# Kernel tuning notes

Measured on AMD Instinct MI355X. Metric: run time of the kernel, lower is better.

The kernel has to match this reference:

```python
import jax, jax.numpy as jnp
import numpy as np

N, IN_DIM, OUT_DIM, BATCH = 8192, 128, 128, 4


def _glorot(key, shape):
    lim = float(np.sqrt(6.0 / (shape[0] + shape[1])))
    return jax.random.uniform(key, shape, jnp.float32, -lim, lim)


def setup_inputs() -> dict:
    key = jax.random.key(0)
    ks = jax.random.split(key, 16)
    inp = {
        "x": jax.random.normal(ks[0], (BATCH, N, IN_DIM), jnp.float32),
        "L0": jax.random.normal(ks[1], (N, N), jnp.float32) / np.sqrt(N),
        "L1": jax.random.normal(ks[2], (N, N), jnp.float32) / np.sqrt(N),
        "L2": jax.random.normal(ks[3], (N, N), jnp.float32) / np.sqrt(N),
        "L3": jax.random.normal(ks[4], (N, N), jnp.float32) / np.sqrt(N),
    }
    # 8 GCN layers: (branch b, layer l) -> W_bl, bias_bl
    kidx = 5
    for b in range(4):
        for l in range(2):
            d_in = IN_DIM if l == 0 else OUT_DIM
            inp[f"W{b}{l}"] = _glorot(ks[kidx], (d_in, OUT_DIM))
            inp[f"b{b}{l}"] = jnp.zeros((OUT_DIM,), jnp.float32)
            kidx += 1
    return inp


def _gcn_block(L, x, W, b):
    # support = L @ x  (graph propagation), then dense transform + ReLU
    support = jnp.einsum("nm,bmf->bnf", L, x)  # [B, N, F_in]
    return jax.nn.relu(support @ W + b)        # [B, N, F_out]


def reference(x, L0, L1, L2, L3,
              W00, b00, W01, b01,
              W10, b10, W11, b11,
              W20, b20, W21, b21,
              W30, b30, W31, b31):
    x0 = _gcn_block(L0, _gcn_block(L0, x, W00, b00), W01, b01)
    x1 = _gcn_block(L1, _gcn_block(L1, x, W10, b10), W11, b11)
    x2 = _gcn_block(L2, _gcn_block(L2, x, W20, b20), W21, b21)
    x3 = _gcn_block(L3, _gcn_block(L3, x, W30, b30), W31, b31)
    return (x0, x1, x2, x3)
```

## Files before the change

### kernel.cpp

```cpp
#include <hip/hip_runtime.h>
#include <stdint.h>


typedef short bf16x8 __attribute__((ext_vector_type(8)));
typedef float f32x4  __attribute__((ext_vector_type(4)));
typedef float f32x16 __attribute__((ext_vector_type(16)));

static __device__ __forceinline__ unsigned short f2bf(float f) {
  __bf16 h = (__bf16)f;
  return __builtin_bit_cast(unsigned short, h);
}
static __device__ __forceinline__ unsigned int pack2(float a, float b) {
  return (unsigned int)f2bf(a) | ((unsigned int)f2bf(b) << 16);
}
static __device__ __forceinline__ bf16x8 cvt8(float4 lo, float4 hi) {
  bf16x8 r;
  r[0] = (short)f2bf(lo.x); r[1] = (short)f2bf(lo.y);
  r[2] = (short)f2bf(lo.z); r[3] = (short)f2bf(lo.w);
  r[4] = (short)f2bf(hi.x); r[5] = (short)f2bf(hi.y);
  r[6] = (short)f2bf(hi.z); r[7] = (short)f2bf(hi.w);
  return r;
}

#define GLOAD16(g, l)                                                                  \
  __builtin_amdgcn_global_load_lds((const __attribute__((address_space(1))) void*)(g), \
                                   (__attribute__((address_space(3))) void*)(l), 16, 0, 0)

struct WPtrs { const float* w[8]; };
__global__ __launch_bounds__(256)
void prep_w(WPtrs p, unsigned short* __restrict__ wt) {
  const int s = blockIdx.x;
  const float* W = p.w[s];
  unsigned short* dst = wt + s * 16384;
  for (int i = threadIdx.x; i < 16384; i += 256) {
    const int fi = i >> 7, fo = i & 127;
    dst[fo * 128 + fi] = f2bf(W[i]);
  }
}

struct LPtrs { const float* l[4]; };
__global__ __launch_bounds__(256)
void conv_l(LPtrs p, char* __restrict__ lbf) {
  __shared__ char T[65536];
  const int t = threadIdx.x, lane = t & 63, wave = t >> 6;
  const int rg = blockIdx.x, kg = blockIdx.y, br = blockIdx.z;
  const float* L = p.l[br];
  const int r0 = rg * 64, k0 = kg * 512;
  const int mt = rg >> 2, rowoff = (rg & 3) * 64, kt0 = kg * 16;
#pragma unroll
  for (int i = 0; i < 16; ++i) {
    const int rr = wave * 16 + i;
    const float* src = L + (size_t)(r0 + rr) * 8192 + k0;
#pragma unroll
    for (int half = 0; half < 2; ++half) {
      float4 v = ((const float4*)src)[half * 64 + lane];
      const int ktl = half * 8 + (lane >> 3);
      const int ch  = ((lane >> 1) & 3) ^ ((rr >> 1) & 3);
      uint2 pv; pv.x = pack2(v.x, v.y); pv.y = pack2(v.z, v.w);
      *(uint2*)(T + ktl * 4096 + rr * 64 + ch * 16 + (lane & 1) * 8) = pv;
    }
  }
  __syncthreads();
  char* dstb = lbf + ((size_t)(br * 32 + mt) * 256 + kt0) * 16384 + rowoff * 64;
#pragma unroll
  for (int ktl = 0; ktl < 16; ++ktl)
    ((uint4*)(dstb + (size_t)ktl * 16384))[t] = ((const uint4*)(T + ktl * 4096))[t];
}

template <int AFP32>
__global__ __launch_bounds__(256)
void small_gemm(const float* __restrict__ x, const unsigned short* __restrict__ H1m,
                const unsigned short* __restrict__ WT, unsigned short* __restrict__ Z) {
  __shared__ unsigned short Sa[128 * 136];

  const int t = threadIdx.x, lane = t & 63, wave = t >> 6;
  const int l15 = lane & 15, lk = (lane >> 4) * 8;
  const int wm = (wave >> 1) * 64, wn = (wave & 1) * 64;
  const int mt = blockIdx.x, br = blockIdx.y;
  const int batch = mt >> 6, node0 = (mt & 63) * 128;

  {
    const int row = t >> 1, seg = (t & 1) * 64;
    if (AFP32) {
      const float4* src = (const float4*)(x + ((size_t)batch * 8192 + node0 + row) * 128 + seg);
      uint4* dst = (uint4*)&Sa[row * 136 + seg];
#pragma unroll
      for (int i = 0; i < 8; ++i) {
        float4 a = src[i * 2], b = src[i * 2 + 1];
        uint4 v;
        v.x = pack2(a.x, a.y); v.y = pack2(a.z, a.w);
        v.z = pack2(b.x, b.y); v.w = pack2(b.z, b.w);
        dst[i] = v;
      }
    } else {
      const uint4* src = (const uint4*)(H1m + ((size_t)(br * 4 + batch) * 8192 + node0 + row) * 128 + seg);
      uint4* dst = (uint4*)&Sa[row * 136 + seg];
#pragma unroll
      for (int i = 0; i < 8; ++i) dst[i] = src[i];
    }
  }
  __syncthreads();

  const unsigned short* WTb = WT + (size_t)(2 * br + (AFP32 ? 0 : 1)) * 16384;
  f32x4 acc[4][4];
#pragma unroll
  for (int i = 0; i < 4; ++i)
#pragma unroll
    for (int j = 0; j < 4; ++j) acc[i][j] = f32x4{0.f, 0.f, 0.f, 0.f};

#pragma unroll
  for (int kk = 0; kk < 4; ++kk) {
    bf16x8 av[4], wv[4];
#pragma unroll
    for (int mi = 0; mi < 4; ++mi)
      av[mi] = *(const bf16x8*)&Sa[(wm + mi * 16 + l15) * 136 + kk * 32 + lk];
#pragma unroll
    for (int ni = 0; ni < 4; ++ni)
      wv[ni] = *(const bf16x8*)&WTb[(wn + ni * 16 + l15) * 128 + kk * 32 + lk];
#pragma unroll
    for (int mi = 0; mi < 4; ++mi)
#pragma unroll
      for (int ni = 0; ni < 4; ++ni)
        acc[mi][ni] = __builtin_amdgcn_mfma_f32_16x16x32_bf16(av[mi], wv[ni], acc[mi][ni], 0, 0, 0);
  }

#pragma unroll
  for (int mi = 0; mi < 4; ++mi) {
#pragma unroll
    for (int ni = 0; ni < 4; ++ni) {
      const int row0 = wm + mi * 16 + (lane >> 4) * 4;
      const int col  = wn + ni * 16 + l15;
      uint2 pv;
      pv.x = pack2(acc[mi][ni][0], acc[mi][ni][1]);
      pv.y = pack2(acc[mi][ni][2], acc[mi][ni][3]);
      *(uint2*)(Z + ((size_t)br * 512 + batch * 128 + col) * 8192 + node0 + row0) = pv;
    }
  }
}

struct BigArgs {
  const float* L[4];
  const float* bias[4];
  const unsigned short* Z;
  void* Dst;
};

#define DO_MFMA() do {                                                       \
    __builtin_amdgcn_s_setprio(1);                                           \
    c00 = __builtin_amdgcn_mfma_f32_32x32x16_bf16(av0, bv0, c00, 0, 0, 0);   \
    c01 = __builtin_amdgcn_mfma_f32_32x32x16_bf16(av0, bv1, c01, 0, 0, 0);   \
    c10 = __builtin_amdgcn_mfma_f32_32x32x16_bf16(av1, bv0, c10, 0, 0, 0);   \
    c11 = __builtin_amdgcn_mfma_f32_32x32x16_bf16(av1, bv1, c11, 0, 0, 0);   \
    c20 = __builtin_amdgcn_mfma_f32_32x32x16_bf16(av2, bv0, c20, 0, 0, 0);   \
    c21 = __builtin_amdgcn_mfma_f32_32x32x16_bf16(av2, bv1, c21, 0, 0, 0);   \
    c30 = __builtin_amdgcn_mfma_f32_32x32x16_bf16(av3, bv0, c30, 0, 0, 0);   \
    c31 = __builtin_amdgcn_mfma_f32_32x32x16_bf16(av3, bv1, c31, 0, 0, 0);   \
    __builtin_amdgcn_s_setprio(0); } while (0)

#define RD(ab_, bb_, s_) do {                                          \
    const int _ch = ((2 * (s_) + hk) ^ key4) * 16;                     \
    av0 = *(const bf16x8*)((ab_) + aBase + _ch);                       \
    av1 = *(const bf16x8*)((ab_) + aBase + 2048 + _ch);                \
    av2 = *(const bf16x8*)((ab_) + aBase + 4096 + _ch);                \
    av3 = *(const bf16x8*)((ab_) + aBase + 6144 + _ch);                \
    bv0 = *(const bf16x8*)((bb_) + bBase + _ch);                       \
    bv1 = *(const bf16x8*)((bb_) + bBase + 2048 + _ch); } while (0)

#define BIG_EPILOGUE()                                                                     \
  __syncthreads();                                                                          \
  if (LAYER == 0) {                                                                         \
    unsigned short* S16 = (unsigned short*)smem;                                            \
    _Pragma("unroll")                                                                       \
    for (int h = 0; h < 2; ++h) {                                                           \
      if (((wave >> 1) & 1) == h) {                                                         \
        EPI16(0, 0, c00); EPI16(0, 1, c01);                                                 \
        EPI16(1, 0, c10); EPI16(1, 1, c11);                                                 \
        EPI16(2, 0, c20); EPI16(2, 1, c21);                                                 \
        EPI16(3, 0, c30); EPI16(3, 1, c31);                                                 \
      }                                                                                     \
      __syncthreads();                                                                      \
      const int batch = nb * 2 + h;                                                         \
      const int row = t >> 1, seg = (t & 1) * 64;                                           \
      unsigned short* Dst = (unsigned short*)a.Dst;                                         \
      const uint4* src = (const uint4*)&S16[row * 136 + seg];                               \
      uint4* dst = (uint4*)(Dst + ((size_t)(br * 4 + batch) * 8192 + mbase + row) * 128 + seg); \
      _Pragma("unroll") for (int i = 0; i < 8; ++i) dst[i] = src[i];                        \
      __syncthreads();                                                                      \
    }                                                                                       \
  } else {                                                                                  \
    float* S32 = (float*)smem;                                                              \
    _Pragma("unroll")                                                                       \
    for (int h = 0; h < 2; ++h) {                                                           \
      _Pragma("unroll")                                                                     \
      for (int rh = 0; rh < 2; ++rh) {                                                      \
        if (((wave >> 1) & 1) == h && (wave >> 2) == rh) {                                  \
          EPI32(0, 0, c00); EPI32(0, 1, c01);                                               \
          EPI32(1, 0, c10); EPI32(1, 1, c11);                                               \
          EPI32(2, 0, c20); EPI32(2, 1, c21);                                               \
          EPI32(3, 0, c30); EPI32(3, 1, c31);                                               \
        }                                                                                   \
        __syncthreads();                                                                    \
        const int batch = nb * 2 + h;                                                       \
        const int row = t >> 2, seg = (t & 3) * 32;                                         \
        float* Dst = (float*)a.Dst;                                                         \
        const float4* src = (const float4*)&S32[row * 128 + seg];                           \
        float4* dst = (float4*)(Dst + ((size_t)(br * 4 + batch) * 8192 + mbase + rh * 128 + row) * 128 + seg); \
        _Pragma("unroll") for (int i = 0; i < 8; ++i) dst[i] = src[i];                      \
        __syncthreads();                                                                    \
      }                                                                                     \
    }                                                                                       \
  }

#define EPI16(AM, BN, ACC) do {                                             \
    const int col = (wave & 1) * 64 + (BN) * 32 + l31;                      \
    const float bvv = bias[col];                                            \
    _Pragma("unroll") for (int r = 0; r < 16; ++r) {                        \
      const int row = wm + (AM) * 32 + (r & 3) + 8 * (r >> 2) + 4 * hk;     \
      S16[row * 136 + col] = f2bf(fmaxf(ACC[r] + bvv, 0.f));                \
    } } while (0)
#define EPI32(AM, BN, ACC) do {                                             \
    const int col = (wave & 1) * 64 + (BN) * 32 + l31;                      \
    const float bvv = bias[col];                                            \
    _Pragma("unroll") for (int r = 0; r < 16; ++r) {                        \
      const int lrow = (AM) * 32 + (r & 3) + 8 * (r >> 2) + 4 * hk;         \
      S32[lrow * 128 + col] = fmaxf(ACC[r] + bvv, 0.f);                     \
    } } while (0)

template <int LAYER>
__global__ __launch_bounds__(512)
void big_gemm_pc(BigArgs a, const char* __restrict__ Lbf) {
  extern __shared__ char smem[];

  const int t = threadIdx.x, lane = t & 63, wave = t >> 6;
  const int l31 = lane & 31, hk = lane >> 5;
  const int wm = (wave >> 2) * 128, wn = (wave & 3) * 64;

  const int bid = blockIdx.x;
  const int work = (bid & 7) * 32 + (bid >> 3);
  const int nb = work & 1, mt = (work >> 1) & 31, br = work >> 6;
  const int mbase = mt * 256;

  const float* bias = a.bias[br];
  const unsigned short* Zb = a.Z + (size_t)br * (512 * 8192);

  const char* aTiles = Lbf + ((size_t)(br * 32 + mt) * 256) * 16384;
  const unsigned short* bG = Zb + (size_t)(nb * 256 + wave * 32 + (lane >> 2)) * 8192
                                + ((lane & 3) ^ ((lane >> 3) & 3)) * 8;

  const int aBase = (wm + l31) * 64;
  const int bBase = (wn + l31) * 64;
  const int key4 = (l31 >> 1) & 3;

  f32x16 c00{}, c01{}, c10{}, c11{}, c20{}, c21{}, c30{}, c31{};
  bf16x8 av0, av1, av2, av3, bv0, bv1;

#define STG(T_) do {                                                          \
    const char* _as = aTiles + (size_t)(T_) * 16384 + wave * 2048 + lane * 16;\
    char* _ad = smem + ((T_) & 3) * 16384 + wave * 2048;                      \
    GLOAD16(_as, _ad);                                                        \
    GLOAD16(_as + 1024, _ad + 1024);                                          \
    const unsigned short* _bp = bG + (size_t)(T_) * 32;                       \
    char* _bl = smem + 65536 + ((T_) & 3) * 16384 + wave * 2048;              \
    GLOAD16(_bp, _bl);                                                        \
    GLOAD16(_bp + 16 * 8192, _bl + 1024); } while (0)

#define ITER(T_, VMSTR, DO_STG) do {                                          \
    asm volatile("s_waitcnt " VMSTR ::: "memory");                            \
    __builtin_amdgcn_s_barrier();                                             \
    if (DO_STG) STG((T_) + 3);                                                \
    const char* _ab = smem + ((T_) & 3) * 16384;                              \
    const char* _bb = smem + 65536 + ((T_) & 3) * 16384;                      \
    RD(_ab, _bb, 0);                                                          \
    DO_MFMA();                                                                \
    RD(_ab, _bb, 1);                                                          \
    DO_MFMA();                                                                \
  } while (0)

  STG(0); STG(1); STG(2);

  for (int T = 0; T < 252; T += 4) {
    ITER(T,     "vmcnt(8)", 1);
    ITER(T + 1, "vmcnt(8)", 1);
    ITER(T + 2, "vmcnt(8)", 1);
    ITER(T + 3, "vmcnt(8)", 1);
  }
  ITER(252, "vmcnt(8)", 1);
  ITER(253, "vmcnt(8)", 0);
  ITER(254, "vmcnt(4)", 0);
  ITER(255, "vmcnt(0)", 0);
#undef ITER
#undef STG

  BIG_EPILOGUE()
}

template <int LAYER>
__global__ __launch_bounds__(512, 2)
void big_gemm_rs(BigArgs a) {
  extern __shared__ char smem[];

  const int t = threadIdx.x, lane = t & 63, wave = t >> 6;
  const int l31 = lane & 31, hk = lane >> 5;
  const int wm = (wave >> 2) * 128, wn = (wave & 3) * 64;

  const int bid = blockIdx.x;
  const int work = (bid & 7) * 32 + (bid >> 3);
  const int nb = work & 1, mt = (work >> 1) & 31, br = work >> 6;
  const int mbase = mt * 256;

  const float* A = a.L[br];
  const float* bias = a.bias[br];
  const unsigned short* Zb = a.Z + (size_t)br * (512 * 8192);

  const int arow = t >> 1, ah = t & 1;
  const float* aG = A + (size_t)(mbase + arow) * 8192 + ah * 16;
  const int c0 = 2 * ah, akey = (arow >> 1) & 3;
  char* aRowL = smem + arow * 64;
  const unsigned short* bG = Zb + (size_t)(nb * 256 + wave * 32 + (lane >> 2)) * 8192
                                + ((lane & 3) ^ ((lane >> 3) & 3)) * 8;
  char* bWave = smem + 32768 + wave * 2048;

  const int aBase = (wm + l31) * 64;
  const int bBase = (wn + l31) * 64;
  const int key4 = (l31 >> 1) & 3;

  f32x16 c00{}, c01{}, c10{}, c11{}, c20{}, c21{}, c30{}, c31{};
  float4 s0[4], s1[4], s2[4];
  bf16x8 av0, av1, av2, av3, bv0, bv1;

#define GLB(T_) do {                                                   \
    const unsigned short* _bp = bG + (size_t)(T_) * 32;                \
    char* _bl = bWave + ((T_) & 3) * 16384;                            \
    GLOAD16(_bp, _bl);                                                 \
    GLOAD16(_bp + 16 * 8192, _bl + 1024); } while (0)
#define LOADA(T_, R) do {                                              \
    const float* _ap = aG + (size_t)(T_) * 32;                         \
    R[0] = *(const float4*)(_ap);                                      \
    R[1] = *(const float4*)(_ap + 4);                                  \
    R[2] = *(const float4*)(_ap + 8);                                  \
    R[3] = *(const float4*)(_ap + 12); } while (0)
#define WRITEA(T_, R) do {                                             \
    char* _al = aRowL + (((T_) & 1)) * 16384;                          \
    *(bf16x8*)(_al + ((c0 ^ akey) * 16))       = cvt8(R[0], R[1]);     \
    *(bf16x8*)(_al + (((c0 + 1) ^ akey) * 16)) = cvt8(R[2], R[3]); } while (0)
#define ITER(T_, SLOAD, SWRITE, VMSTR, DO_STAGE, DO_WRITE) do {        \
    asm volatile("s_waitcnt " VMSTR ::: "memory");                     \
    asm volatile("s_waitcnt lgkmcnt(0)" ::: "memory");                 \
    __builtin_amdgcn_s_barrier();                                      \
    if (DO_STAGE) { GLB((T_) + 3); LOADA((T_) + 3, SLOAD); }           \
    const char* _ab = smem + ((T_) & 1) * 16384;                       \
    const char* _bb = smem + 32768 + ((T_) & 3) * 16384;               \
    RD(_ab, _bb, 0);                                                   \
    DO_MFMA();                                                         \
    if (DO_WRITE) WRITEA((T_) + 1, SWRITE);                            \
    RD(_ab, _bb, 1);                                                   \
    DO_MFMA();                                                         \
  } while (0)

  GLB(0); LOADA(0, s0);
  GLB(1); LOADA(1, s1);
  GLB(2); LOADA(2, s2);
  WRITEA(0, s0);

  for (int T = 0; T < 252; T += 3) {
    ITER(T,     s0, s1, "vmcnt(12)", 1, 1);
    ITER(T + 1, s1, s2, "vmcnt(12)", 1, 1);
    ITER(T + 2, s2, s0, "vmcnt(12)", 1, 1);
  }
  ITER(252, s0, s1, "vmcnt(12)", 1, 1);
  ITER(253, s0, s2, "vmcnt(12)", 0, 1);
  ITER(254, s0, s0, "vmcnt(6)",  0, 1);
  ITER(255, s0, s0, "vmcnt(0)",  0, 0);
#undef ITER
#undef WRITEA
#undef LOADA
#undef GLB

  BIG_EPILOGUE()
}

extern "C" void kernel_launch(void* const* d_in, const int* in_sizes, int n_in,
                              void* d_out, int out_size, void* d_ws, size_t ws_size,
                              hipStream_t stream) {
  const float* x = (const float*)d_in[0];
  unsigned short* Z   = (unsigned short*)d_ws;
  unsigned short* H1m = Z + (size_t)4 * 512 * 8192;
  unsigned short* WT  = H1m + (size_t)4 * 4 * 8192 * 128;
  char* Lbf = (char*)(WT + 8 * 16384);
  float* out = (float*)d_out;

  const size_t NEED_PC = (size_t)33554432 + 33554432 + 262144 + 536870912;
  const bool use_pc = ws_size >= NEED_PC;

  static int attr_done = 0;
  if (!attr_done) {
    hipFuncSetAttribute((const void*)big_gemm_pc<0>, hipFuncAttributeMaxDynamicSharedMemorySize, 131072);
    hipFuncSetAttribute((const void*)big_gemm_pc<1>, hipFuncAttributeMaxDynamicSharedMemorySize, 131072);
    hipFuncSetAttribute((const void*)big_gemm_rs<0>, hipFuncAttributeMaxDynamicSharedMemorySize, 98304);
    hipFuncSetAttribute((const void*)big_gemm_rs<1>, hipFuncAttributeMaxDynamicSharedMemorySize, 98304);
    attr_done = 1;
  }

  WPtrs wp;
  for (int b = 0; b < 4; ++b) {
    wp.w[b * 2 + 0] = (const float*)d_in[5 + b * 4 + 0];
    wp.w[b * 2 + 1] = (const float*)d_in[5 + b * 4 + 2];
  }
  prep_w<<<8, 256, 0, stream>>>(wp, WT);

  BigArgs a0, a1;
  for (int b = 0; b < 4; ++b) {
    a0.L[b] = (const float*)d_in[1 + b];
    a1.L[b] = (const float*)d_in[1 + b];
    a0.bias[b] = (const float*)d_in[6 + b * 4];
    a1.bias[b] = (const float*)d_in[8 + b * 4];
  }
  a0.Z = Z; a0.Dst = (void*)H1m;
  a1.Z = Z; a1.Dst = (void*)out;

  if (use_pc) {
    LPtrs lp;
    for (int b = 0; b < 4; ++b) lp.l[b] = (const float*)d_in[1 + b];
    conv_l<<<dim3(128, 16, 4), 256, 0, stream>>>(lp, Lbf);
    small_gemm<1><<<dim3(256, 4), 256, 0, stream>>>(x, nullptr, WT, Z);
    big_gemm_pc<0><<<256, 512, 131072, stream>>>(a0, Lbf);
    small_gemm<0><<<dim3(256, 4), 256, 0, stream>>>(nullptr, H1m, WT, Z);
    big_gemm_pc<1><<<256, 512, 131072, stream>>>(a1, Lbf);
  } else {
    small_gemm<1><<<dim3(256, 4), 256, 0, stream>>>(x, nullptr, WT, Z);
    big_gemm_rs<0><<<256, 512, 98304, stream>>>(a0);
    small_gemm<0><<<dim3(256, 4), 256, 0, stream>>>(nullptr, H1m, WT, Z);
    big_gemm_rs<1><<<256, 512, 98304, stream>>>(a1);
  }
}
```

Measured before the change: 934.8 us.

## Shrink L conversion tiles, use nontemporal access, and double-buffer MFMA operand reads

The L fp32-to-bf16 conversion kernel now handles half as many columns per block, with twice as many blocks and half the LDS. It uses nontemporal loads and stores so the streamed L data does not pollute the cache. In the big GEMM kernels, both k-substeps' LDS operands go into separate register sets; in the pc variant both reads are issued before the MFMAs, to hide LDS latency. This costs more VGPRs and may lower occupancy.

```diff
diff --git a/kernel.cpp b/kernel.cpp
--- a/kernel.cpp
+++ b/kernel.cpp
@@ -4,6 +4,7 @@
 
 typedef short bf16x8 __attribute__((ext_vector_type(8)));
 typedef float f32x4  __attribute__((ext_vector_type(4)));
+typedef unsigned int u32x4 __attribute__((ext_vector_type(4)));
 typedef float f32x16 __attribute__((ext_vector_type(16)));
 
 static __device__ __forceinline__ unsigned short f2bf(float f) {
@@ -41,30 +42,29 @@
 struct LPtrs { const float* l[4]; };
 __global__ __launch_bounds__(256)
 void conv_l(LPtrs p, char* __restrict__ lbf) {
-  __shared__ char T[65536];
+  __shared__ char T[32768];
   const int t = threadIdx.x, lane = t & 63, wave = t >> 6;
   const int rg = blockIdx.x, kg = blockIdx.y, br = blockIdx.z;
   const float* L = p.l[br];
-  const int r0 = rg * 64, k0 = kg * 512;
-  const int mt = rg >> 2, rowoff = (rg & 3) * 64, kt0 = kg * 16;
+  const int r0 = rg * 64, k0 = kg * 256;
+  const int mt = rg >> 2, rowoff = (rg & 3) * 64, kt0 = kg * 8;
 #pragma unroll
   for (int i = 0; i < 16; ++i) {
     const int rr = wave * 16 + i;
-    const float* src = L + (size_t)(r0 + rr) * 8192 + k0;
-#pragma unroll
-    for (int half = 0; half < 2; ++half) {
-      float4 v = ((const float4*)src)[half * 64 + lane];
-      const int ktl = half * 8 + (lane >> 3);
-      const int ch  = ((lane >> 1) & 3) ^ ((rr >> 1) & 3);
-      uint2 pv; pv.x = pack2(v.x, v.y); pv.y = pack2(v.z, v.w);
-      *(uint2*)(T + ktl * 4096 + rr * 64 + ch * 16 + (lane & 1) * 8) = pv;
-    }
+    const f32x4* src = (const f32x4*)(L + (size_t)(r0 + rr) * 8192 + k0);
+    f32x4 v = __builtin_nontemporal_load(src + lane);
+    const int ktl = lane >> 3;
+    const int ch  = ((lane >> 1) & 3) ^ ((rr >> 1) & 3);
+    uint2 pv; pv.x = pack2(v[0], v[1]); pv.y = pack2(v[2], v[3]);
+    *(uint2*)(T + ktl * 4096 + rr * 64 + ch * 16 + (lane & 1) * 8) = pv;
   }
   __syncthreads();
   char* dstb = lbf + ((size_t)(br * 32 + mt) * 256 + kt0) * 16384 + rowoff * 64;
 #pragma unroll
-  for (int ktl = 0; ktl < 16; ++ktl)
-    ((uint4*)(dstb + (size_t)ktl * 16384))[t] = ((const uint4*)(T + ktl * 4096))[t];
+  for (int ktl = 0; ktl < 8; ++ktl) {
+    u32x4 v = ((const u32x4*)(T + ktl * 4096))[t];
+    __builtin_nontemporal_store(v, (u32x4*)(dstb + (size_t)ktl * 16384) + t);
+  }
 }
 
 template <int AFP32>
@@ -145,26 +145,26 @@
   void* Dst;
 };
 
-#define DO_MFMA() do {                                                       \
+#define MFMASET(AV0, AV1, AV2, AV3, BV0, BV1) do {                           \
     __builtin_amdgcn_s_setprio(1);                                           \
-    c00 = __builtin_amdgcn_mfma_f32_32x32x16_bf16(av0, bv0, c00, 0, 0, 0);   \
-    c01 = __builtin_amdgcn_mfma_f32_32x32x16_bf16(av0, bv1, c01, 0, 0, 0);   \
-    c10 = __builtin_amdgcn_mfma_f32_32x32x16_bf16(av1, bv0, c10, 0, 0, 0);   \
-    c11 = __builtin_amdgcn_mfma_f32_32x32x16_bf16(av1, bv1, c11, 0, 0, 0);   \
-    c20 = __builtin_amdgcn_mfma_f32_32x32x16_bf16(av2, bv0, c20, 0, 0, 0);   \
-    c21 = __builtin_amdgcn_mfma_f32_32x32x16_bf16(av2, bv1, c21, 0, 0, 0);   \
-    c30 = __builtin_amdgcn_mfma_f32_32x32x16_bf16(av3, bv0, c30, 0, 0, 0);   \
-    c31 = __builtin_amdgcn_mfma_f32_32x32x16_bf16(av3, bv1, c31, 0, 0, 0);   \
+    c00 = __builtin_amdgcn_mfma_f32_32x32x16_bf16(AV0, BV0, c00, 0, 0, 0);   \
+    c01 = __builtin_amdgcn_mfma_f32_32x32x16_bf16(AV0, BV1, c01, 0, 0, 0);   \
+    c10 = __builtin_amdgcn_mfma_f32_32x32x16_bf16(AV1, BV0, c10, 0, 0, 0);   \
+    c11 = __builtin_amdgcn_mfma_f32_32x32x16_bf16(AV1, BV1, c11, 0, 0, 0);   \
+    c20 = __builtin_amdgcn_mfma_f32_32x32x16_bf16(AV2, BV0, c20, 0, 0, 0);   \
+    c21 = __builtin_amdgcn_mfma_f32_32x32x16_bf16(AV2, BV1, c21, 0, 0, 0);   \
+    c30 = __builtin_amdgcn_mfma_f32_32x32x16_bf16(AV3, BV0, c30, 0, 0, 0);   \
+    c31 = __builtin_amdgcn_mfma_f32_32x32x16_bf16(AV3, BV1, c31, 0, 0, 0);   \
     __builtin_amdgcn_s_setprio(0); } while (0)
 
-#define RD(ab_, bb_, s_) do {                                          \
+#define RDSET(ab_, bb_, s_, AV0, AV1, AV2, AV3, BV0, BV1) do {         \
     const int _ch = ((2 * (s_) + hk) ^ key4) * 16;                     \
-    av0 = *(const bf16x8*)((ab_) + aBase + _ch);                       \
-    av1 = *(const bf16x8*)((ab_) + aBase + 2048 + _ch);                \
-    av2 = *(const bf16x8*)((ab_) + aBase + 4096 + _ch);                \
-    av3 = *(const bf16x8*)((ab_) + aBase + 6144 + _ch);                \
-    bv0 = *(const bf16x8*)((bb_) + bBase + _ch);                       \
-    bv1 = *(const bf16x8*)((bb_) + bBase + 2048 + _ch); } while (0)
+    AV0 = *(const bf16x8*)((ab_) + aBase + _ch);                       \
+    AV1 = *(const bf16x8*)((ab_) + aBase + 2048 + _ch);                \
+    AV2 = *(const bf16x8*)((ab_) + aBase + 4096 + _ch);                \
+    AV3 = *(const bf16x8*)((ab_) + aBase + 6144 + _ch);                \
+    BV0 = *(const bf16x8*)((bb_) + bBase + _ch);                       \
+    BV1 = *(const bf16x8*)((bb_) + bBase + 2048 + _ch); } while (0)
 
 #define BIG_EPILOGUE()                                                                     \
   __syncthreads();                                                                          \
@@ -252,7 +252,8 @@
   const int key4 = (l31 >> 1) & 3;
 
   f32x16 c00{}, c01{}, c10{}, c11{}, c20{}, c21{}, c30{}, c31{};
-  bf16x8 av0, av1, av2, av3, bv0, bv1;
+  bf16x8 pa0, pa1, pa2, pa3, pb0, pb1;
+  bf16x8 qa0, qa1, qa2, qa3, qb0, qb1;
 
 #define STG(T_) do {                                                          \
     const char* _as = aTiles + (size_t)(T_) * 16384 + wave * 2048 + lane * 16;\
@@ -270,10 +271,10 @@
     if (DO_STG) STG((T_) + 3);                                                \
     const char* _ab = smem + ((T_) & 3) * 16384;                              \
     const char* _bb = smem + 65536 + ((T_) & 3) * 16384;                      \
-    RD(_ab, _bb, 0);                                                          \
-    DO_MFMA();                                                                \
-    RD(_ab, _bb, 1);                                                          \
-    DO_MFMA();                                                                \
+    RDSET(_ab, _bb, 0, pa0, pa1, pa2, pa3, pb0, pb1);                         \
+    RDSET(_ab, _bb, 1, qa0, qa1, qa2, qa3, qb0, qb1);                         \
+    MFMASET(pa0, pa1, pa2, pa3, pb0, pb1);                                    \
+    MFMASET(qa0, qa1, qa2, qa3, qb0, qb1);                                    \
   } while (0)
 
   STG(0); STG(1); STG(2);
@@ -326,7 +327,8 @@
 
   f32x16 c00{}, c01{}, c10{}, c11{}, c20{}, c21{}, c30{}, c31{};
   float4 s0[4], s1[4], s2[4];
-  bf16x8 av0, av1, av2, av3, bv0, bv1;
+  bf16x8 pa0, pa1, pa2, pa3, pb0, pb1;
+  bf16x8 qa0, qa1, qa2, qa3, qb0, qb1;
 
 #define GLB(T_) do {                                                   \
     const unsigned short* _bp = bG + (size_t)(T_) * 32;                \
@@ -350,11 +352,11 @@
     if (DO_STAGE) { GLB((T_) + 3); LOADA((T_) + 3, SLOAD); }           \
     const char* _ab = smem + ((T_) & 1) * 16384;                       \
     const char* _bb = smem + 32768 + ((T_) & 3) * 16384;               \
-    RD(_ab, _bb, 0);                                                   \
-    DO_MFMA();                                                         \
+    RDSET(_ab, _bb, 0, pa0, pa1, pa2, pa3, pb0, pb1);                  \
+    MFMASET(pa0, pa1, pa2, pa3, pb0, pb1);                             \
     if (DO_WRITE) WRITEA((T_) + 1, SWRITE);                            \
-    RD(_ab, _bb, 1);                                                   \
-    DO_MFMA();                                                         \
+    RDSET(_ab, _bb, 1, qa0, qa1, qa2, qa3, qb0, qb1);                  \
+    MFMASET(qa0, qa1, qa2, qa3, qb0, qb1);                             \
   } while (0)
 
   GLB(0); LOADA(0, s0);
@@ -394,10 +396,10 @@
 
   static int attr_done = 0;
   if (!attr_done) {
-    hipFuncSetAttribute((const void*)big_gemm_pc<0>, hipFuncAttributeMaxDynamicSharedMemorySize, 131072);
-    hipFuncSetAttribute((const void*)big_gemm_pc<1>, hipFuncAttributeMaxDynamicSharedMemorySize, 131072);
-    hipFuncSetAttribute((const void*)big_gemm_rs<0>, hipFuncAttributeMaxDynamicSharedMemorySize, 98304);
-    hipFuncSetAttribute((const void*)big_gemm_rs<1>, hipFuncAttributeMaxDynamicSharedMemorySize, 98304);
+    (void)hipFuncSetAttribute((const void*)big_gemm_pc<0>, hipFuncAttributeMaxDynamicSharedMemorySize, 131072);
+    (void)hipFuncSetAttribute((const void*)big_gemm_pc<1>, hipFuncAttributeMaxDynamicSharedMemorySize, 131072);
+    (void)hipFuncSetAttribute((const void*)big_gemm_rs<0>, hipFuncAttributeMaxDynamicSharedMemorySize, 98304);
+    (void)hipFuncSetAttribute((const void*)big_gemm_rs<1>, hipFuncAttributeMaxDynamicSharedMemorySize, 98304);
     attr_done = 1;
   }
 
@@ -421,7 +423,7 @@
   if (use_pc) {
     LPtrs lp;
     for (int b = 0; b < 4; ++b) lp.l[b] = (const float*)d_in[1 + b];
-    conv_l<<<dim3(128, 16, 4), 256, 0, stream>>>(lp, Lbf);
+    conv_l<<<dim3(128, 32, 4), 256, 0, stream>>>(lp, Lbf);
     small_gemm<1><<<dim3(256, 4), 256, 0, stream>>>(x, nullptr, WT, Z);
     big_gemm_pc<0><<<256, 512, 131072, stream>>>(a0, Lbf);
     small_gemm<0><<<dim3(256, 4), 256, 0, stream>>>(nullptr, H1m, WT, Z);
```

After: 924.6 us. Within noise of the previous version (-1.1%).
